# Kernel optimization log

Measured on AMD Instinct MI355X. Metric: run time of the kernel, lower is better.

Reference implementation:

```python
import jax, jax.numpy as jnp
import numpy as np

B, S, D, H = 2, 2048, 1024, 16
HD = D // H  # head_dim = 64


def setup_inputs() -> dict:
    key = jax.random.key(0)
    k1, k2, k3, k4, k5 = jax.random.split(key, 5)
    x = jax.random.normal(k1, (B, S, D), dtype=jnp.float32)
    # causal additive mask [S, S]: 0 on/below diagonal, -1e9 above
    mask = jnp.where(jnp.tril(jnp.ones((S, S), dtype=bool)), 0.0, -1e9).astype(jnp.float32)
    scale = 1.0 / np.sqrt(D)
    W_qkv = jax.random.normal(k2, (D, 3 * D), dtype=jnp.float32) * scale
    b_qkv = jax.random.normal(k3, (3 * D,), dtype=jnp.float32) * 0.01
    W_o = jax.random.normal(k4, (D, D), dtype=jnp.float32) * scale
    b_o = jax.random.normal(k5, (D,), dtype=jnp.float32) * 0.01
    return {"x": x, "mask": mask, "W_qkv": W_qkv, "b_qkv": b_qkv, "W_o": W_o, "b_o": b_o}


def reference(x, mask, W_qkv, b_qkv, W_o, b_o):
    b, s, d = x.shape
    qkv = x @ W_qkv + b_qkv                         # [B,S,3D]
    qkv = qkv.reshape(b, s, H, 3 * HD).transpose(0, 2, 1, 3)  # [B,H,S,3*HD]
    q, k, v = jnp.split(qkv, 3, axis=-1)            # each [B,H,S,HD]
    scores = jnp.einsum('bhqd,bhkd->bhqk', q, k) / np.sqrt(HD)  # [B,H,S,S]
    scores = scores + mask                           # broadcast [S,S] additive mask
    attn = jax.nn.softmax(scores, axis=-1)
    vals = jnp.einsum('bhqk,bhkd->bhqd', attn, v)    # [B,H,S,HD]
    vals = vals.transpose(0, 2, 1, 3).reshape(b, s, d)
    return vals @ W_o + b_o
```

## Files before the change

kernel.cpp:

```cpp
#include <hip/hip_runtime.h>

#define NB 2
#define NS 2048
#define ND 1024
#define NH 16
#define NHD 64
#define QLD (3 * ND)
#define PADP 72
#define PADV 68

typedef unsigned short u16;
typedef __attribute__((ext_vector_type(8))) short short8;
typedef __attribute__((ext_vector_type(4))) short short4v;
typedef __attribute__((ext_vector_type(4))) float f32x4;

__device__ __forceinline__ u16 f2b(float f) {
    unsigned int x = __float_as_uint(f);
    return (u16)((x + 0x7fffu + ((x >> 16) & 1u)) >> 16);
}

__global__ __launch_bounds__(256) void convert_bf16(
    const float* __restrict__ src, u16* __restrict__ dst, int n)
{
    const int i = (blockIdx.x * 256 + threadIdx.x) * 8;
    if (i >= n) return;
    float4 a = *(const float4*)(src + i);
    float4 b = *(const float4*)(src + i + 4);
    *(ushort4*)(dst + i)     = make_ushort4(f2b(a.x), f2b(a.y), f2b(a.z), f2b(a.w));
    *(ushort4*)(dst + i + 4) = make_ushort4(f2b(b.x), f2b(b.y), f2b(b.z), f2b(b.w));
}

__global__ __launch_bounds__(256) void transpose_bf16(
    const float* __restrict__ W, u16* __restrict__ WT, int K, int N)
{
    __shared__ u16 Ts[64 * 72];
    const int t = threadIdx.x;
    const int k0 = blockIdx.y << 6, n0 = blockIdx.x << 6;
    const int r = t >> 4, c = (t & 15) << 2;
    #pragma unroll
    for (int rr = 0; rr < 64; rr += 16) {
        float4 v = *(const float4*)&W[(size_t)(k0 + r + rr) * N + n0 + c];
        Ts[(c + 0) * 72 + r + rr] = f2b(v.x);
        Ts[(c + 1) * 72 + r + rr] = f2b(v.y);
        Ts[(c + 2) * 72 + r + rr] = f2b(v.z);
        Ts[(c + 3) * 72 + r + rr] = f2b(v.w);
    }
    __syncthreads();
    const int n = t >> 2, cc = (t & 3) << 4;
    uint4 a = *(const uint4*)&Ts[n * 72 + cc];
    uint4 b = *(const uint4*)&Ts[n * 72 + cc + 8];
    *(uint4*)&WT[(size_t)(n0 + n) * K + k0 + cc]     = a;
    *(uint4*)&WT[(size_t)(n0 + n) * K + k0 + cc + 8] = b;
}

template <bool STORE_BF16>
__global__ __launch_bounds__(256) void gemm_mfma(
    const u16* __restrict__ A, const u16* __restrict__ BT,
    const float* __restrict__ bias,
    void* __restrict__ C, int M, int N, int K)
{
    __shared__ u16 As[128 * 32];
    __shared__ u16 Bs[128 * 32];

    const int tid = threadIdx.x;
    const int wave = tid >> 6, lane = tid & 63;
    const int col = lane & 15, quad = lane >> 4;
    const int wm = wave >> 1, wn = wave & 1;
    const int row0 = blockIdx.y << 7, col0 = blockIdx.x << 7;

    f32x4 acc[4][4] = {};

    const u16* asrc[2];
    const u16* bsrc[2];
    u16* adst[2];
    u16* bdst[2];
    #pragma unroll
    for (int is = 0; is < 2; ++is) {
        const int J = is * 256 + wave * 64 + lane;
        const int m = J >> 2;
        const int q = (J & 3) ^ ((m >> 1) & 3);
        asrc[is] = A  + (size_t)(row0 + m) * K + q * 8;
        bsrc[is] = BT + (size_t)(col0 + m) * K + q * 8;
        adst[is] = &As[(size_t)(is * 256 + wave * 64) * 8];
        bdst[is] = &Bs[(size_t)(is * 256 + wave * 64) * 8];
    }

    for (int kk = 0; kk < K; kk += 32) {
        __syncthreads();
        #pragma unroll
        for (int is = 0; is < 2; ++is) {
            __builtin_amdgcn_global_load_lds(
                (const __attribute__((address_space(1))) unsigned int*)(asrc[is] + kk),
                (__attribute__((address_space(3))) unsigned int*)adst[is], 16, 0, 0);
            __builtin_amdgcn_global_load_lds(
                (const __attribute__((address_space(1))) unsigned int*)(bsrc[is] + kk),
                (__attribute__((address_space(3))) unsigned int*)bdst[is], 16, 0, 0);
        }
        __syncthreads();

        short8 af[4], bf[4];
        #pragma unroll
        for (int i = 0; i < 4; ++i) {
            const int m = wm * 64 + i * 16 + col;
            af[i] = *(const short8*)&As[(m * 4 + (quad ^ ((m >> 1) & 3))) * 8];
        }
        #pragma unroll
        for (int j = 0; j < 4; ++j) {
            const int n = wn * 64 + j * 16 + col;
            bf[j] = *(const short8*)&Bs[(n * 4 + (quad ^ ((n >> 1) & 3))) * 8];
        }
        #pragma unroll
        for (int i = 0; i < 4; ++i)
            #pragma unroll
            for (int j = 0; j < 4; ++j)
                acc[i][j] = __builtin_amdgcn_mfma_f32_16x16x32_bf16(
                    af[i], bf[j], acc[i][j], 0, 0, 0);
    }

    #pragma unroll
    for (int j = 0; j < 4; ++j) {
        const int gc = col0 + wn * 64 + j * 16 + col;
        const float bj = bias[gc];
        #pragma unroll
        for (int i = 0; i < 4; ++i) {
            const int gr = row0 + wm * 64 + i * 16 + quad * 4;
            #pragma unroll
            for (int r = 0; r < 4; ++r) {
                const float v = acc[i][j][r] + bj;
                if (STORE_BF16)
                    ((u16*)C)[(size_t)(gr + r) * N + gc] = f2b(v);
                else
                    ((float*)C)[(size_t)(gr + r) * N + gc] = v;
            }
        }
    }
}

__global__ __launch_bounds__(256) void attn_kernel(
    const u16* __restrict__ qkv, u16* __restrict__ vals)
{
    __shared__ u16 Ks[64 * 64];
    __shared__ u16 Vt[64 * PADV];
    __shared__ u16 Ps[64 * PADP];

    const int tid = threadIdx.x;
    const int wave = tid >> 6, lane = tid & 63;
    const int col = lane & 15, quad = lane >> 4;
    const int qtA = blockIdx.x;
    const int qtB = 31 - qtA;
    const int bh = blockIdx.y;
    const int b = bh >> 4, h = bh & 15;
    const size_t base = (size_t)b * NS * QLD + (size_t)h * (3 * NHD);
    const int q0 = wave * 16;

    int Jrow[2], Jcol[2];
    u16* kdst[2];
    #pragma unroll
    for (int is = 0; is < 2; ++is) {
        const int J = is * 256 + wave * 64 + lane;
        Jrow[is] = J >> 3;
        Jcol[is] = (((J & 7) ^ (Jrow[is] & 7))) << 3;
        kdst[is] = &Ks[(size_t)(is * 256 + wave * 64) * 8];
    }

    auto stage_tile = [&](int srow, int coloff) {
        #pragma unroll
        for (int is = 0; is < 2; ++is) {
            __builtin_amdgcn_global_load_lds(
                (const __attribute__((address_space(1))) unsigned int*)
                    (qkv + base + (size_t)(srow + Jrow[is]) * QLD + coloff + Jcol[is]),
                (__attribute__((address_space(3))) unsigned int*)kdst[is], 16, 0, 0);
        }
    };
    auto read_frag = [&](int row, int half) -> short8 {
        const int blk = row * 8 + (((quad + (half << 2))) ^ (row & 7));
        return *(const short8*)&Ks[blk << 3];
    };

    stage_tile(qtA * 64, 0);
    __syncthreads();
    short8 aqA0 = read_frag(q0 + col, 0);
    short8 aqA1 = read_frag(q0 + col, 1);
    __syncthreads();
    stage_tile(qtB * 64, 0);
    __syncthreads();
    short8 aqB0 = read_frag(q0 + col, 0);
    short8 aqB1 = read_frag(q0 + col, 1);

    f32x4 accA[4] = {}, accB[4] = {};
    float mA[4], lA[4], mB[4], lB[4];
    #pragma unroll
    for (int r = 0; r < 4; ++r) { mA[r] = mB[r] = -1e30f; lA[r] = lB[r] = 0.f; }

    auto process = [&](const short8& a0, const short8& a1,
                       f32x4* accO, float* mrow, float* lrow, bool diag) {
        f32x4 s[4] = {};
        #pragma unroll
        for (int kg = 0; kg < 4; ++kg) {
            short8 b0 = read_frag(kg * 16 + col, 0);
            short8 b1 = read_frag(kg * 16 + col, 1);
            s[kg] = __builtin_amdgcn_mfma_f32_16x16x32_bf16(a0, b0, s[kg], 0, 0, 0);
            s[kg] = __builtin_amdgcn_mfma_f32_16x16x32_bf16(a1, b1, s[kg], 0, 0, 0);
        }
        #pragma unroll
        for (int kg = 0; kg < 4; ++kg)
            #pragma unroll
            for (int r = 0; r < 4; ++r) {
                float v = s[kg][r] * 0.125f;
                if (diag && (kg * 16 + col > q0 + quad * 4 + r)) v = -1e30f;
                s[kg][r] = v;
            }
        float alpha[4];
        #pragma unroll
        for (int r = 0; r < 4; ++r) {
            float mx = fmaxf(fmaxf(s[0][r], s[1][r]), fmaxf(s[2][r], s[3][r]));
            mx = fmaxf(mx, __shfl_xor(mx, 1, 64));
            mx = fmaxf(mx, __shfl_xor(mx, 2, 64));
            mx = fmaxf(mx, __shfl_xor(mx, 4, 64));
            mx = fmaxf(mx, __shfl_xor(mx, 8, 64));
            float mn = fmaxf(mrow[r], mx);
            alpha[r] = __expf(mrow[r] - mn);
            mrow[r] = mn;
        }
        #pragma unroll
        for (int r = 0; r < 4; ++r) {
            float ps = 0.f;
            #pragma unroll
            for (int kg = 0; kg < 4; ++kg) {
                float p = __expf(s[kg][r] - mrow[r]);
                ps += p;
                Ps[(q0 + quad * 4 + r) * PADP + kg * 16 + col] = f2b(p);
            }
            ps += __shfl_xor(ps, 1, 64);
            ps += __shfl_xor(ps, 2, 64);
            ps += __shfl_xor(ps, 4, 64);
            ps += __shfl_xor(ps, 8, 64);
            lrow[r] = lrow[r] * alpha[r] + ps;
            #pragma unroll
            for (int dg = 0; dg < 4; ++dg) accO[dg][r] *= alpha[r];
        }
        short8 ap0 = *(const short8*)&Ps[(q0 + col) * PADP + quad * 8];
        short8 ap1 = *(const short8*)&Ps[(q0 + col) * PADP + 32 + quad * 8];
        #pragma unroll
        for (int dg = 0; dg < 4; ++dg) {
            const int n = dg * 16 + col;
            short4v lo0 = *(const short4v*)&Vt[n * PADV + quad * 8];
            short4v hi0 = *(const short4v*)&Vt[n * PADV + quad * 8 + 4];
            short4v lo1 = *(const short4v*)&Vt[n * PADV + 32 + quad * 8];
            short4v hi1 = *(const short4v*)&Vt[n * PADV + 32 + quad * 8 + 4];
            short8 b0 = __builtin_shufflevector(lo0, hi0, 0, 1, 2, 3, 4, 5, 6, 7);
            short8 b1 = __builtin_shufflevector(lo1, hi1, 0, 1, 2, 3, 4, 5, 6, 7);
            accO[dg] = __builtin_amdgcn_mfma_f32_16x16x32_bf16(ap0, b0, accO[dg], 0, 0, 0);
            accO[dg] = __builtin_amdgcn_mfma_f32_16x16x32_bf16(ap1, b1, accO[dg], 0, 0, 0);
        }
    };

    for (int kt = 0; kt <= qtB; ++kt) {
        __syncthreads();
        stage_tile(kt * 64, NHD);
        {
            const int tx = tid & 15, ty = tid >> 4;
            const int k0 = ty << 2, d0 = tx << 2;
            const u16* vsrc = qkv + base + (size_t)(kt * 64 + k0) * QLD + 2 * NHD + d0;
            ushort4 r0 = *(const ushort4*)(vsrc);
            ushort4 r1 = *(const ushort4*)(vsrc + QLD);
            ushort4 r2 = *(const ushort4*)(vsrc + 2 * QLD);
            ushort4 r3 = *(const ushort4*)(vsrc + 3 * QLD);
            *(ushort4*)&Vt[(d0 + 0) * PADV + k0] = make_ushort4(r0.x, r1.x, r2.x, r3.x);
            *(ushort4*)&Vt[(d0 + 1) * PADV + k0] = make_ushort4(r0.y, r1.y, r2.y, r3.y);
            *(ushort4*)&Vt[(d0 + 2) * PADV + k0] = make_ushort4(r0.z, r1.z, r2.z, r3.z);
            *(ushort4*)&Vt[(d0 + 3) * PADV + k0] = make_ushort4(r0.w, r1.w, r2.w, r3.w);
        }
        __syncthreads();

        process(aqB0, aqB1, accB, mB, lB, kt == qtB);
        if (kt <= qtA)
            process(aqA0, aqA1, accA, mA, lA, kt == qtA);
    }

    #pragma unroll
    for (int r = 0; r < 4; ++r) {
        const float invA = 1.f / lA[r];
        const float invB = 1.f / lB[r];
        const size_t rowA = ((size_t)b * NS + qtA * 64 + q0 + quad * 4 + r) * ND + h * NHD;
        const size_t rowB = ((size_t)b * NS + qtB * 64 + q0 + quad * 4 + r) * ND + h * NHD;
        #pragma unroll
        for (int dg = 0; dg < 4; ++dg) {
            vals[rowA + dg * 16 + col] = f2b(accA[dg][r] * invA);
            vals[rowB + dg * 16 + col] = f2b(accB[dg][r] * invB);
        }
    }
}

extern "C" void kernel_launch(void* const* d_in, const int* in_sizes, int n_in,
                              void* d_out, int out_size, void* d_ws, size_t ws_size,
                              hipStream_t stream)
{
    const float* x    = (const float*)d_in[0];
    const float* Wqkv = (const float*)d_in[2];
    const float* bqkv = (const float*)d_in[3];
    const float* Wo   = (const float*)d_in[4];
    const float* bo   = (const float*)d_in[5];
    float* out = (float*)d_out;

    u16* x_bf   = (u16*)d_ws;
    u16* WqkvT  = x_bf   + (size_t)4096 * 1024;
    u16* WoT    = WqkvT  + (size_t)3072 * 1024;
    u16* qkv    = WoT    + (size_t)1024 * 1024;
    u16* vals   = qkv    + (size_t)4096 * 3072;

    const int M = NB * NS;

    convert_bf16<<<dim3(M * ND / (256 * 8)), dim3(256), 0, stream>>>(
        x, x_bf, M * ND);
    transpose_bf16<<<dim3(QLD / 64, ND / 64), dim3(256), 0, stream>>>(
        Wqkv, WqkvT, ND, QLD);
    transpose_bf16<<<dim3(ND / 64, ND / 64), dim3(256), 0, stream>>>(
        Wo, WoT, ND, ND);

    gemm_mfma<true><<<dim3(QLD / 128, M / 128), dim3(256), 0, stream>>>(
        x_bf, WqkvT, bqkv, qkv, M, QLD, ND);
    attn_kernel<<<dim3(16, NB * NH), dim3(256), 0, stream>>>(qkv, vals);
    gemm_mfma<false><<<dim3(ND / 128, M / 128), dim3(256), 0, stream>>>(
        vals, WoT, bo, out, M, ND, ND);
}
```

Baseline: 238.0 us.

## Double-buffer K/V tiles and prefetch next tile during attention compute

Adds two LDS buffers for K and transposed V and issues the async load of the next K tile and the register load of the next V tile before computing on the current tile. K and V fragments are read once into registers per tile and shared between the paired query tiles, instead of being re-read from LDS in each process call. The aim is to hide global-load latency behind MFMA work and to cut duplicated LDS reads. In exchange it uses more LDS and many more registers for the kb/vb fragments and the prefetched V, which may lower occupancy, and it keeps two barriers per iteration.

```diff
diff --git a/kernel.cpp b/kernel.cpp
--- a/kernel.cpp
+++ b/kernel.cpp
@@ -139,8 +139,8 @@
 __global__ __launch_bounds__(256) void attn_kernel(
     const u16* __restrict__ qkv, u16* __restrict__ vals)
 {
-    __shared__ u16 Ks[64 * 64];
-    __shared__ u16 Vt[64 * PADV];
+    __shared__ u16 Ks[2][64 * 64];
+    __shared__ u16 Vt[2][64 * PADV];
     __shared__ u16 Ps[64 * PADP];
 
     const int tid = threadIdx.x;
@@ -154,38 +154,58 @@
     const int q0 = wave * 16;
 
     int Jrow[2], Jcol[2];
-    u16* kdst[2];
     #pragma unroll
     for (int is = 0; is < 2; ++is) {
         const int J = is * 256 + wave * 64 + lane;
         Jrow[is] = J >> 3;
-        Jcol[is] = (((J & 7) ^ (Jrow[is] & 7))) << 3;
-        kdst[is] = &Ks[(size_t)(is * 256 + wave * 64) * 8];
-    }
-
-    auto stage_tile = [&](int srow, int coloff) {
+        Jcol[is] = ((J & 7) ^ (Jrow[is] & 7)) << 3;
+    }
+
+    auto stage_tile = [&](int buf, int srow, int coloff) {
         #pragma unroll
         for (int is = 0; is < 2; ++is) {
             __builtin_amdgcn_global_load_lds(
                 (const __attribute__((address_space(1))) unsigned int*)
                     (qkv + base + (size_t)(srow + Jrow[is]) * QLD + coloff + Jcol[is]),
-                (__attribute__((address_space(3))) unsigned int*)kdst[is], 16, 0, 0);
-        }
-    };
-    auto read_frag = [&](int row, int half) -> short8 {
-        const int blk = row * 8 + (((quad + (half << 2))) ^ (row & 7));
-        return *(const short8*)&Ks[blk << 3];
-    };
-
-    stage_tile(qtA * 64, 0);
-    __syncthreads();
-    short8 aqA0 = read_frag(q0 + col, 0);
-    short8 aqA1 = read_frag(q0 + col, 1);
-    __syncthreads();
-    stage_tile(qtB * 64, 0);
-    __syncthreads();
-    short8 aqB0 = read_frag(q0 + col, 0);
-    short8 aqB1 = read_frag(q0 + col, 1);
+                (__attribute__((address_space(3))) unsigned int*)
+                    &Ks[buf][(size_t)(is * 256 + wave * 64) * 8], 16, 0, 0);
+        }
+    };
+    auto read_frag = [&](int buf, int row, int half) -> short8 {
+        const int blk = row * 8 + ((quad + (half << 2)) ^ (row & 7));
+        return *(const short8*)&Ks[buf][blk << 3];
+    };
+
+    const int vtx = tid & 15, vty = tid >> 4;
+    const int vk0 = vty << 2, vd0 = vtx << 2;
+    auto load_vregs = [&](int kt, ushort4* vr) {
+        const u16* vsrc = qkv + base + (size_t)(kt * 64 + vk0) * QLD + 2 * NHD + vd0;
+        vr[0] = *(const ushort4*)(vsrc);
+        vr[1] = *(const ushort4*)(vsrc + QLD);
+        vr[2] = *(const ushort4*)(vsrc + 2 * QLD);
+        vr[3] = *(const ushort4*)(vsrc + 3 * QLD);
+    };
+    auto write_vt = [&](int buf, const ushort4* vr) {
+        *(ushort4*)&Vt[buf][(vd0 + 0) * PADV + vk0] =
+            make_ushort4(vr[0].x, vr[1].x, vr[2].x, vr[3].x);
+        *(ushort4*)&Vt[buf][(vd0 + 1) * PADV + vk0] =
+            make_ushort4(vr[0].y, vr[1].y, vr[2].y, vr[3].y);
+        *(ushort4*)&Vt[buf][(vd0 + 2) * PADV + vk0] =
+            make_ushort4(vr[0].z, vr[1].z, vr[2].z, vr[3].z);
+        *(ushort4*)&Vt[buf][(vd0 + 3) * PADV + vk0] =
+            make_ushort4(vr[0].w, vr[1].w, vr[2].w, vr[3].w);
+    };
+
+    stage_tile(0, qtA * 64, 0);
+    __syncthreads();
+    short8 aqA0 = read_frag(0, q0 + col, 0);
+    short8 aqA1 = read_frag(0, q0 + col, 1);
+    __syncthreads();
+    stage_tile(0, qtB * 64, 0);
+    __syncthreads();
+    short8 aqB0 = read_frag(0, q0 + col, 0);
+    short8 aqB1 = read_frag(0, q0 + col, 1);
+    __syncthreads();
 
     f32x4 accA[4] = {}, accB[4] = {};
     float mA[4], lA[4], mB[4], lB[4];
@@ -193,14 +213,13 @@
     for (int r = 0; r < 4; ++r) { mA[r] = mB[r] = -1e30f; lA[r] = lB[r] = 0.f; }
 
     auto process = [&](const short8& a0, const short8& a1,
+                       short8 (*kb)[2], short8 (*vb)[2],
                        f32x4* accO, float* mrow, float* lrow, bool diag) {
         f32x4 s[4] = {};
         #pragma unroll
         for (int kg = 0; kg < 4; ++kg) {
-            short8 b0 = read_frag(kg * 16 + col, 0);
-            short8 b1 = read_frag(kg * 16 + col, 1);
-            s[kg] = __builtin_amdgcn_mfma_f32_16x16x32_bf16(a0, b0, s[kg], 0, 0, 0);
-            s[kg] = __builtin_amdgcn_mfma_f32_16x16x32_bf16(a1, b1, s[kg], 0, 0, 0);
+            s[kg] = __builtin_amdgcn_mfma_f32_16x16x32_bf16(a0, kb[kg][0], s[kg], 0, 0, 0);
+            s[kg] = __builtin_amdgcn_mfma_f32_16x16x32_bf16(a1, kb[kg][1], s[kg], 0, 0, 0);
         }
         #pragma unroll
         for (int kg = 0; kg < 4; ++kg)
@@ -243,39 +262,49 @@
         short8 ap1 = *(const short8*)&Ps[(q0 + col) * PADP + 32 + quad * 8];
         #pragma unroll
         for (int dg = 0; dg < 4; ++dg) {
+            accO[dg] = __builtin_amdgcn_mfma_f32_16x16x32_bf16(ap0, vb[dg][0], accO[dg], 0, 0, 0);
+            accO[dg] = __builtin_amdgcn_mfma_f32_16x16x32_bf16(ap1, vb[dg][1], accO[dg], 0, 0, 0);
+        }
+    };
+
+    ushort4 vcur[4], vnxt[4];
+    stage_tile(0, 0, NHD);
+    load_vregs(0, vcur);
+
+    for (int kt = 0; kt <= qtB; ++kt) {
+        const int cur = kt & 1, nxt = cur ^ 1;
+        __syncthreads();
+        write_vt(cur, vcur);
+        __syncthreads();
+
+        if (kt < qtB) {
+            stage_tile(nxt, (kt + 1) * 64, NHD);
+            load_vregs(kt + 1, vnxt);
+        }
+
+        short8 kb[4][2], vb[4][2];
+        #pragma unroll
+        for (int kg = 0; kg < 4; ++kg) {
+            kb[kg][0] = read_frag(cur, kg * 16 + col, 0);
+            kb[kg][1] = read_frag(cur, kg * 16 + col, 1);
+        }
+        #pragma unroll
+        for (int dg = 0; dg < 4; ++dg) {
             const int n = dg * 16 + col;
-            short4v lo0 = *(const short4v*)&Vt[n * PADV + quad * 8];
-            short4v hi0 = *(const short4v*)&Vt[n * PADV + quad * 8 + 4];
-            short4v lo1 = *(const short4v*)&Vt[n * PADV + 32 + quad * 8];
-            short4v hi1 = *(const short4v*)&Vt[n * PADV + 32 + quad * 8 + 4];
-            short8 b0 = __builtin_shufflevector(lo0, hi0, 0, 1, 2, 3, 4, 5, 6, 7);
-            short8 b1 = __builtin_shufflevector(lo1, hi1, 0, 1, 2, 3, 4, 5, 6, 7);
-            accO[dg] = __builtin_amdgcn_mfma_f32_16x16x32_bf16(ap0, b0, accO[dg], 0, 0, 0);
-            accO[dg] = __builtin_amdgcn_mfma_f32_16x16x32_bf16(ap1, b1, accO[dg], 0, 0, 0);
-        }
-    };
-
-    for (int kt = 0; kt <= qtB; ++kt) {
-        __syncthreads();
-        stage_tile(kt * 64, NHD);
-        {
-            const int tx = tid & 15, ty = tid >> 4;
-            const int k0 = ty << 2, d0 = tx << 2;
-            const u16* vsrc = qkv + base + (size_t)(kt * 64 + k0) * QLD + 2 * NHD + d0;
-            ushort4 r0 = *(const ushort4*)(vsrc);
-            ushort4 r1 = *(const ushort4*)(vsrc + QLD);
-            ushort4 r2 = *(const ushort4*)(vsrc + 2 * QLD);
-            ushort4 r3 = *(const ushort4*)(vsrc + 3 * QLD);
-            *(ushort4*)&Vt[(d0 + 0) * PADV + k0] = make_ushort4(r0.x, r1.x, r2.x, r3.x);
-            *(ushort4*)&Vt[(d0 + 1) * PADV + k0] = make_ushort4(r0.y, r1.y, r2.y, r3.y);
-            *(ushort4*)&Vt[(d0 + 2) * PADV + k0] = make_ushort4(r0.z, r1.z, r2.z, r3.z);
-            *(ushort4*)&Vt[(d0 + 3) * PADV + k0] = make_ushort4(r0.w, r1.w, r2.w, r3.w);
-        }
-        __syncthreads();
-
-        process(aqB0, aqB1, accB, mB, lB, kt == qtB);
+            short4v lo0 = *(const short4v*)&Vt[cur][n * PADV + quad * 8];
+            short4v hi0 = *(const short4v*)&Vt[cur][n * PADV + quad * 8 + 4];
+            short4v lo1 = *(const short4v*)&Vt[cur][n * PADV + 32 + quad * 8];
+            short4v hi1 = *(const short4v*)&Vt[cur][n * PADV + 32 + quad * 8 + 4];
+            vb[dg][0] = __builtin_shufflevector(lo0, hi0, 0, 1, 2, 3, 4, 5, 6, 7);
+            vb[dg][1] = __builtin_shufflevector(lo1, hi1, 0, 1, 2, 3, 4, 5, 6, 7);
+        }
+
+        process(aqB0, aqB1, kb, vb, accB, mB, lB, kt == qtB);
         if (kt <= qtA)
-            process(aqA0, aqA1, accA, mA, lA, kt == qtA);
+            process(aqA0, aqA1, kb, vb, accA, mA, lA, kt == qtA);
+
+        #pragma unroll
+        for (int i = 0; i < 4; ++i) vcur[i] = vnxt[i];
     }
 
     #pragma unroll
```

After: 238.1 us. No clear change (+0.1%).

## Split paired causal q-tiles into separate blocks and transpose MFMA operand roles

Applied to the files above, without the earlier changes.

The attention kernel no longer pairs q-tile i with tile 31-i in one block. It launches 32 blocks per (batch, head), each handling a single q-tile, which gives more independent blocks but leaves the causal work unbalanced across blocks. The MFMA operands are swapped so each lane owns one query row. The softmax max and sum reductions then need only two cross-lane shuffles, and the output is written as packed ushort4 stores. Each block now reloads K and V for only one tile's lifetime, so there is less K/V reuse per load than with the pair.

```diff
diff --git a/kernel.cpp b/kernel.cpp
--- a/kernel.cpp
+++ b/kernel.cpp
@@ -146,21 +146,19 @@
     const int tid = threadIdx.x;
     const int wave = tid >> 6, lane = tid & 63;
     const int col = lane & 15, quad = lane >> 4;
-    const int qtA = blockIdx.x;
-    const int qtB = 31 - qtA;
+    const int qt = 31 - blockIdx.x;
     const int bh = blockIdx.y;
     const int b = bh >> 4, h = bh & 15;
     const size_t base = (size_t)b * NS * QLD + (size_t)h * (3 * NHD);
     const int q0 = wave * 16;
+    const int qloc = q0 + col;
 
     int Jrow[2], Jcol[2];
-    u16* kdst[2];
     #pragma unroll
     for (int is = 0; is < 2; ++is) {
         const int J = is * 256 + wave * 64 + lane;
         Jrow[is] = J >> 3;
-        Jcol[is] = (((J & 7) ^ (Jrow[is] & 7))) << 3;
-        kdst[is] = &Ks[(size_t)(is * 256 + wave * 64) * 8];
+        Jcol[is] = ((J & 7) ^ (Jrow[is] & 7)) << 3;
     }
 
     auto stage_tile = [&](int srow, int coloff) {
@@ -169,78 +167,92 @@
             __builtin_amdgcn_global_load_lds(
                 (const __attribute__((address_space(1))) unsigned int*)
                     (qkv + base + (size_t)(srow + Jrow[is]) * QLD + coloff + Jcol[is]),
-                (__attribute__((address_space(3))) unsigned int*)kdst[is], 16, 0, 0);
+                (__attribute__((address_space(3))) unsigned int*)
+                    &Ks[(size_t)(is * 256 + wave * 64) * 8], 16, 0, 0);
         }
     };
     auto read_frag = [&](int row, int half) -> short8 {
-        const int blk = row * 8 + (((quad + (half << 2))) ^ (row & 7));
+        const int blk = row * 8 + ((quad + (half << 2)) ^ (row & 7));
         return *(const short8*)&Ks[blk << 3];
     };
 
-    stage_tile(qtA * 64, 0);
+    stage_tile(qt * 64, 0);
     __syncthreads();
-    short8 aqA0 = read_frag(q0 + col, 0);
-    short8 aqA1 = read_frag(q0 + col, 1);
-    __syncthreads();
-    stage_tile(qtB * 64, 0);
-    __syncthreads();
-    short8 aqB0 = read_frag(q0 + col, 0);
-    short8 aqB1 = read_frag(q0 + col, 1);
-
-    f32x4 accA[4] = {}, accB[4] = {};
-    float mA[4], lA[4], mB[4], lB[4];
-    #pragma unroll
-    for (int r = 0; r < 4; ++r) { mA[r] = mB[r] = -1e30f; lA[r] = lB[r] = 0.f; }
-
-    auto process = [&](const short8& a0, const short8& a1,
-                       f32x4* accO, float* mrow, float* lrow, bool diag) {
+    short8 bq0 = read_frag(qloc, 0);
+    short8 bq1 = read_frag(qloc, 1);
+
+    f32x4 accO[4] = {};
+    float m = -1e30f, l = 0.f;
+
+    const int vtx = tid & 15, vty = tid >> 4;
+    const int vk0 = vty << 2, vd0 = vtx << 2;
+
+    for (int kt = 0; kt <= qt; ++kt) {
+        __syncthreads();
+        stage_tile(kt * 64, NHD);
+        {
+            const u16* vsrc = qkv + base + (size_t)(kt * 64 + vk0) * QLD + 2 * NHD + vd0;
+            ushort4 r0 = *(const ushort4*)(vsrc);
+            ushort4 r1 = *(const ushort4*)(vsrc + QLD);
+            ushort4 r2 = *(const ushort4*)(vsrc + 2 * QLD);
+            ushort4 r3 = *(const ushort4*)(vsrc + 3 * QLD);
+            *(ushort4*)&Vt[(vd0 + 0) * PADV + vk0] = make_ushort4(r0.x, r1.x, r2.x, r3.x);
+            *(ushort4*)&Vt[(vd0 + 1) * PADV + vk0] = make_ushort4(r0.y, r1.y, r2.y, r3.y);
+            *(ushort4*)&Vt[(vd0 + 2) * PADV + vk0] = make_ushort4(r0.z, r1.z, r2.z, r3.z);
+            *(ushort4*)&Vt[(vd0 + 3) * PADV + vk0] = make_ushort4(r0.w, r1.w, r2.w, r3.w);
+        }
+        __syncthreads();
+
         f32x4 s[4] = {};
         #pragma unroll
         for (int kg = 0; kg < 4; ++kg) {
-            short8 b0 = read_frag(kg * 16 + col, 0);
-            short8 b1 = read_frag(kg * 16 + col, 1);
-            s[kg] = __builtin_amdgcn_mfma_f32_16x16x32_bf16(a0, b0, s[kg], 0, 0, 0);
-            s[kg] = __builtin_amdgcn_mfma_f32_16x16x32_bf16(a1, b1, s[kg], 0, 0, 0);
-        }
+            short8 af0 = read_frag(kg * 16 + col, 0);
+            short8 af1 = read_frag(kg * 16 + col, 1);
+            s[kg] = __builtin_amdgcn_mfma_f32_16x16x32_bf16(af0, bq0, s[kg], 0, 0, 0);
+            s[kg] = __builtin_amdgcn_mfma_f32_16x16x32_bf16(af1, bq1, s[kg], 0, 0, 0);
+        }
+
+        const bool diag = (kt == qt);
         #pragma unroll
         for (int kg = 0; kg < 4; ++kg)
             #pragma unroll
             for (int r = 0; r < 4; ++r) {
                 float v = s[kg][r] * 0.125f;
-                if (diag && (kg * 16 + col > q0 + quad * 4 + r)) v = -1e30f;
+                if (diag && (kg * 16 + quad * 4 + r > qloc)) v = -1e30f;
                 s[kg][r] = v;
             }
-        float alpha[4];
-        #pragma unroll
-        for (int r = 0; r < 4; ++r) {
-            float mx = fmaxf(fmaxf(s[0][r], s[1][r]), fmaxf(s[2][r], s[3][r]));
-            mx = fmaxf(mx, __shfl_xor(mx, 1, 64));
-            mx = fmaxf(mx, __shfl_xor(mx, 2, 64));
-            mx = fmaxf(mx, __shfl_xor(mx, 4, 64));
-            mx = fmaxf(mx, __shfl_xor(mx, 8, 64));
-            float mn = fmaxf(mrow[r], mx);
-            alpha[r] = __expf(mrow[r] - mn);
-            mrow[r] = mn;
-        }
-        #pragma unroll
-        for (int r = 0; r < 4; ++r) {
-            float ps = 0.f;
-            #pragma unroll
-            for (int kg = 0; kg < 4; ++kg) {
-                float p = __expf(s[kg][r] - mrow[r]);
+
+        float mx = -1e30f;
+        #pragma unroll
+        for (int kg = 0; kg < 4; ++kg) {
+            float a = fmaxf(fmaxf(s[kg][0], s[kg][1]), fmaxf(s[kg][2], s[kg][3]));
+            mx = fmaxf(mx, a);
+        }
+        mx = fmaxf(mx, __shfl_xor(mx, 16, 64));
+        mx = fmaxf(mx, __shfl_xor(mx, 32, 64));
+        const float mn = fmaxf(m, mx);
+        const float alpha = __expf(m - mn);
+        m = mn;
+
+        float ps = 0.f;
+        #pragma unroll
+        for (int kg = 0; kg < 4; ++kg)
+            #pragma unroll
+            for (int r = 0; r < 4; ++r) {
+                const float p = __expf(s[kg][r] - mn);
                 ps += p;
-                Ps[(q0 + quad * 4 + r) * PADP + kg * 16 + col] = f2b(p);
+                Ps[qloc * PADP + kg * 16 + quad * 4 + r] = f2b(p);
             }
-            ps += __shfl_xor(ps, 1, 64);
-            ps += __shfl_xor(ps, 2, 64);
-            ps += __shfl_xor(ps, 4, 64);
-            ps += __shfl_xor(ps, 8, 64);
-            lrow[r] = lrow[r] * alpha[r] + ps;
-            #pragma unroll
-            for (int dg = 0; dg < 4; ++dg) accO[dg][r] *= alpha[r];
-        }
-        short8 ap0 = *(const short8*)&Ps[(q0 + col) * PADP + quad * 8];
-        short8 ap1 = *(const short8*)&Ps[(q0 + col) * PADP + 32 + quad * 8];
+        ps += __shfl_xor(ps, 16, 64);
+        ps += __shfl_xor(ps, 32, 64);
+        l = l * alpha + ps;
+        #pragma unroll
+        for (int dg = 0; dg < 4; ++dg)
+            #pragma unroll
+            for (int r = 0; r < 4; ++r) accO[dg][r] *= alpha;
+
+        short8 pb0 = *(const short8*)&Ps[qloc * PADP + quad * 8];
+        short8 pb1 = *(const short8*)&Ps[qloc * PADP + 32 + quad * 8];
         #pragma unroll
         for (int dg = 0; dg < 4; ++dg) {
             const int n = dg * 16 + col;
@@ -248,47 +260,23 @@
             short4v hi0 = *(const short4v*)&Vt[n * PADV + quad * 8 + 4];
             short4v lo1 = *(const short4v*)&Vt[n * PADV + 32 + quad * 8];
             short4v hi1 = *(const short4v*)&Vt[n * PADV + 32 + quad * 8 + 4];
-            short8 b0 = __builtin_shufflevector(lo0, hi0, 0, 1, 2, 3, 4, 5, 6, 7);
-            short8 b1 = __builtin_shufflevector(lo1, hi1, 0, 1, 2, 3, 4, 5, 6, 7);
-            accO[dg] = __builtin_amdgcn_mfma_f32_16x16x32_bf16(ap0, b0, accO[dg], 0, 0, 0);
-            accO[dg] = __builtin_amdgcn_mfma_f32_16x16x32_bf16(ap1, b1, accO[dg], 0, 0, 0);
-        }
-    };
-
-    for (int kt = 0; kt <= qtB; ++kt) {
-        __syncthreads();
-        stage_tile(kt * 64, NHD);
-        {
-            const int tx = tid & 15, ty = tid >> 4;
-            const int k0 = ty << 2, d0 = tx << 2;
-            const u16* vsrc = qkv + base + (size_t)(kt * 64 + k0) * QLD + 2 * NHD + d0;
-            ushort4 r0 = *(const ushort4*)(vsrc);
-            ushort4 r1 = *(const ushort4*)(vsrc + QLD);
-            ushort4 r2 = *(const ushort4*)(vsrc + 2 * QLD);
-            ushort4 r3 = *(const ushort4*)(vsrc + 3 * QLD);
-            *(ushort4*)&Vt[(d0 + 0) * PADV + k0] = make_ushort4(r0.x, r1.x, r2.x, r3.x);
-            *(ushort4*)&Vt[(d0 + 1) * PADV + k0] = make_ushort4(r0.y, r1.y, r2.y, r3.y);
-            *(ushort4*)&Vt[(d0 + 2) * PADV + k0] = make_ushort4(r0.z, r1.z, r2.z, r3.z);
-            *(ushort4*)&Vt[(d0 + 3) * PADV + k0] = make_ushort4(r0.w, r1.w, r2.w, r3.w);
-        }
-        __syncthreads();
-
-        process(aqB0, aqB1, accB, mB, lB, kt == qtB);
-        if (kt <= qtA)
-            process(aqA0, aqA1, accA, mA, lA, kt == qtA);
-    }
-
-    #pragma unroll
-    for (int r = 0; r < 4; ++r) {
-        const float invA = 1.f / lA[r];
-        const float invB = 1.f / lB[r];
-        const size_t rowA = ((size_t)b * NS + qtA * 64 + q0 + quad * 4 + r) * ND + h * NHD;
-        const size_t rowB = ((size_t)b * NS + qtB * 64 + q0 + quad * 4 + r) * ND + h * NHD;
-        #pragma unroll
-        for (int dg = 0; dg < 4; ++dg) {
-            vals[rowA + dg * 16 + col] = f2b(accA[dg][r] * invA);
-            vals[rowB + dg * 16 + col] = f2b(accB[dg][r] * invB);
-        }
+            short8 vb0 = __builtin_shufflevector(lo0, hi0, 0, 1, 2, 3, 4, 5, 6, 7);
+            short8 vb1 = __builtin_shufflevector(lo1, hi1, 0, 1, 2, 3, 4, 5, 6, 7);
+            accO[dg] = __builtin_amdgcn_mfma_f32_16x16x32_bf16(vb0, pb0, accO[dg], 0, 0, 0);
+            accO[dg] = __builtin_amdgcn_mfma_f32_16x16x32_bf16(vb1, pb1, accO[dg], 0, 0, 0);
+        }
+    }
+
+    const float inv = 1.f / l;
+    const size_t rowoff = ((size_t)b * NS + qt * 64 + qloc) * ND + h * NHD;
+    #pragma unroll
+    for (int dg = 0; dg < 4; ++dg) {
+        ushort4 o;
+        o.x = f2b(accO[dg][0] * inv);
+        o.y = f2b(accO[dg][1] * inv);
+        o.z = f2b(accO[dg][2] * inv);
+        o.w = f2b(accO[dg][3] * inv);
+        *(ushort4*)(vals + rowoff + dg * 16 + quad * 4) = o;
     }
 }
 
@@ -320,7 +308,7 @@
 
     gemm_mfma<true><<<dim3(QLD / 128, M / 128), dim3(256), 0, stream>>>(
         x_bf, WqkvT, bqkv, qkv, M, QLD, ND);
-    attn_kernel<<<dim3(16, NB * NH), dim3(256), 0, stream>>>(qkv, vals);
+    attn_kernel<<<dim3(32, NB * NH), dim3(256), 0, stream>>>(qkv, vals);
     gemm_mfma<false><<<dim3(ND / 128, M / 128), dim3(256), 0, stream>>>(
         vals, WoT, bo, out, M, ND, ND);
 }
```

Measured after the change: 243.2 us. 1.02x slower.
